# Optimization experiments

Measured on AMD Instinct MI355X. Metric: run time of the kernel, lower is better.

## Reference

```python
import jax, jax.numpy as jnp
import numpy as np
import math
from jax import lax

HIDDEN = 512
BETA = 1.0
MAX_ITERATIONS = 5
CONV_THRESH = 1e-4
SCALE = BETA / math.sqrt(HIDDEN)


def setup_inputs() -> dict:
    key = jax.random.key(0)
    ks = jax.random.split(key, 9)
    B, S, H = 4, 2048, HIDDEN
    w = 1.0 / math.sqrt(H)  # roughly nn.Linear init scale
    return {
        "x": jax.random.normal(ks[0], (B, S, H), jnp.float32),
        "Wq": jax.random.normal(ks[1], (H, H), jnp.float32) * w,
        "bq": jax.random.normal(ks[2], (H,), jnp.float32) * w,
        "Wk": jax.random.normal(ks[3], (H, H), jnp.float32) * w,
        "bk": jax.random.normal(ks[4], (H,), jnp.float32) * w,
        "Wv": jax.random.normal(ks[5], (H, H), jnp.float32) * w,
        "bv": jax.random.normal(ks[6], (H,), jnp.float32) * w,
        "Wo": jax.random.normal(ks[7], (H, H), jnp.float32) * w,
        "bo": jax.random.normal(ks[8], (H,), jnp.float32) * w,
    }


def _hopfield_update(state, keys):
    # scores: [B, S, S]
    scores = jnp.einsum('bsh,bth->bst', state, keys) * SCALE
    attn = jax.nn.softmax(scores, axis=-1)
    return jnp.einsum('bst,bth->bsh', attn, keys)


def reference(x, Wq, bq, Wk, bk, Wv, bv, Wo, bo):
    query = x @ Wq.T + bq
    keys = x @ Wk.T + bk
    values = x @ Wv.T + bv

    # Iterative Hopfield loop: torch breaks after the update that converges.
    # We run a fixed-length scan, freezing state once converged (same math).
    def step(carry, _):
        state, converged, iters = carry
        new_state = _hopfield_update(state, keys)
        # global Frobenius norms, matching torch.norm over the whole tensor
        delta = jnp.linalg.norm(new_state - state) / (jnp.linalg.norm(state) + 1e-8)
        active = jnp.logical_not(converged)
        state = jnp.where(active, new_state, state)
        iters = iters + active.astype(jnp.int32)
        converged = converged | (active & (delta < CONV_THRESH))
        return (state, converged, iters), None

    init = (query, jnp.array(False), jnp.array(0, jnp.int32))
    (state, converged, iterations), _ = lax.scan(step, init, None, length=MAX_ITERATIONS)

    # Final readout attention against values
    scores = jnp.einsum('bsh,bth->bst', state, keys) * SCALE
    attn = jax.nn.softmax(scores, axis=-1)
    out = jnp.einsum('bst,bth->bsh', attn, values)
    out = out @ Wo.T + bo  # dropout p=0.0 / eval: identity
    return out, iterations, converged
```

## Files before the change

kernel.cpp:

```cpp
#include <hip/hip_runtime.h>
#include <hip/hip_bf16.h>
#include <math.h>

#define HH 512
#define BB 4
#define SS 2048
#define NN (BB*SS)
#define SCALE_F 0.04419417382415922f
#define THRESH 1e-4f
#define CTL_FLOATS 1024

typedef __attribute__((ext_vector_type(8))) short bf16x8;
typedef __attribute__((ext_vector_type(4))) float f32x4;

struct Ctl { float sum_d; float sum_o; int iters; int conv; int cur; int bf[10]; };

__device__ __forceinline__ float b2f(unsigned short u) {
    union { unsigned int i; float f; } c; c.i = ((unsigned int)u) << 16; return c.f;
}
__device__ __forceinline__ unsigned short f2b(float f) {
    unsigned int x = __float_as_uint(f);
    unsigned int r = (x + 0x7FFFu + ((x >> 16) & 1u)) >> 16;
    return (unsigned short)r;
}
__device__ __forceinline__ void splitf(float x, unsigned short& h, unsigned short& l) {
    h = f2b(x);
    l = f2b(x - b2f(h));
}
__device__ __forceinline__ f32x4 MF(bf16x8 a, bf16x8 b, f32x4 c) {
    return __builtin_amdgcn_mfma_f32_16x16x32_bf16(a, b, c, 0, 0, 0);
}

typedef __attribute__((address_space(1))) const unsigned int gu32;
typedef __attribute__((address_space(3))) unsigned int lu32;
__device__ __forceinline__ void gl_lds16(const unsigned short* g, unsigned short* l) {
    __builtin_amdgcn_global_load_lds((gu32*)g, (lu32*)l, 16, 0, 0);
}

#define SBAR() do { \
    asm volatile("s_waitcnt vmcnt(0) lgkmcnt(0)" ::: "memory"); \
    __builtin_amdgcn_s_barrier(); \
    asm volatile("" ::: "memory"); \
} while (0)
#define FBAR() do { \
    asm volatile("s_waitcnt lgkmcnt(0)" ::: "memory"); \
    __builtin_amdgcn_s_barrier(); \
    asm volatile("" ::: "memory"); \
} while (0)

__global__ __launch_bounds__(256) void detect_dtypes(
        const void* p0, const void* p1, const void* p2, const void* p3, const void* p4,
        const void* p5, const void* p6, const void* p7, const void* p8, Ctl* sc)
{
    const void* ps[9] = {p0,p1,p2,p3,p4,p5,p6,p7,p8};
    const int   ns[9] = {NN*HH, HH*HH, HH, HH*HH, HH, HH*HH, HH, HH*HH, HH};
    const int i = blockIdx.x;
    const unsigned short* u = (const unsigned short*)ps[i];
    const int n = ns[i] < 4096 ? ns[i] : 4096;
    __shared__ int cnt;
    if (threadIdx.x == 0) cnt = 0;
    __syncthreads();
    int c = 0;
    for (int j = threadIdx.x; j < n; j += 256) {
        const int e = (u[j] >> 7) & 0xFF;
        if (e < 32 || e >= 224) ++c;
    }
    if (c) atomicAdd(&cnt, c);
    __syncthreads();
    if (threadIdx.x == 0) sc->bf[i] = (cnt * 16 < n) ? 1 : 0;
}

__global__ __launch_bounds__(64) void init_flags(Ctl* sc) {
    if (threadIdx.x == 0) {
        sc->iters = 0; sc->conv = 0; sc->cur = 0; sc->sum_d = 0.f; sc->sum_o = 0.f;
        int any = 0;
        for (int i = 0; i < 9; ++i) any |= sc->bf[i];
        sc->bf[9] = any;
    }
}

__global__ __launch_bounds__(256) void mfma_gemm(
    const void* __restrict__ Xv, int xIdx,
    const void* __restrict__ Wv, int wIdx,
    const void* __restrict__ Bv, int bIdx,
    float* __restrict__ outF, void* __restrict__ outExt,
    unsigned short* __restrict__ pKH, unsigned short* __restrict__ pKL,
    unsigned short* __restrict__ pKTH, unsigned short* __restrict__ pKTL,
    float* __restrict__ S0w, float* __restrict__ S1w,
    int mode, const Ctl* __restrict__ sc)
{
    __shared__ unsigned short Xh[64][72], Xl[64][72], Wh[64][72], Wl[64][72];
    const int tid = threadIdx.x;
    const int cur = sc->cur;
    const void* Xp = (xIdx == -2) ? (const void*)(cur ? S1w : S0w) : Xv;
    const bool xbf = (xIdx >= 0) && (sc->bf[xIdx] != 0);
    const bool wbf = (sc->bf[wIdx] != 0);
    const bool bbf = (sc->bf[bIdx] != 0);
    const bool obf = (mode == 1) && (sc->bf[9] != 0);
    const bool xs = !xbf, ws = !wbf;

    const int m0 = blockIdx.x * 64, n0 = blockIdx.y * 64;
    const int lane = tid & 63, w = tid >> 6;
    const int mi = w & 1, ni = w >> 1;
    const int quad = lane >> 4, l16 = lane & 15;
    const int srow = tid >> 2, skb = (tid & 3) * 16;

    f32x4 acc[2][2];
    #pragma unroll
    for (int a = 0; a < 2; ++a)
        #pragma unroll
        for (int bq = 0; bq < 2; ++bq) acc[a][bq] = (f32x4){0.f, 0.f, 0.f, 0.f};

    for (int kc = 0; kc < HH; kc += 64) {
        __syncthreads();
        {
            float v[16];
            if (xbf) {
                const unsigned short* p = (const unsigned short*)Xp + (size_t)(m0 + srow)*HH + kc + skb;
                #pragma unroll
                for (int i = 0; i < 4; ++i) {
                    ushort4 t = *(const ushort4*)(p + 4*i);
                    v[4*i]=b2f(t.x); v[4*i+1]=b2f(t.y); v[4*i+2]=b2f(t.z); v[4*i+3]=b2f(t.w);
                }
            } else {
                const float* p = (const float*)Xp + (size_t)(m0 + srow)*HH + kc + skb;
                #pragma unroll
                for (int i = 0; i < 4; ++i) {
                    float4 t = *(const float4*)(p + 4*i);
                    v[4*i]=t.x; v[4*i+1]=t.y; v[4*i+2]=t.z; v[4*i+3]=t.w;
                }
            }
            #pragma unroll
            for (int i = 0; i < 4; ++i) {
                unsigned short h[4], l[4];
                #pragma unroll
                for (int j = 0; j < 4; ++j) splitf(v[4*i+j], h[j], l[j]);
                *(ushort4*)&Xh[srow][skb + 4*i] = make_ushort4(h[0], h[1], h[2], h[3]);
                if (xs) *(ushort4*)&Xl[srow][skb + 4*i] = make_ushort4(l[0], l[1], l[2], l[3]);
            }
        }
        {
            float v[16];
            if (wbf) {
                const unsigned short* p = (const unsigned short*)Wv + (size_t)(n0 + srow)*HH + kc + skb;
                #pragma unroll
                for (int i = 0; i < 4; ++i) {
                    ushort4 t = *(const ushort4*)(p + 4*i);
                    v[4*i]=b2f(t.x); v[4*i+1]=b2f(t.y); v[4*i+2]=b2f(t.z); v[4*i+3]=b2f(t.w);
                }
            } else {
                const float* p = (const float*)Wv + (size_t)(n0 + srow)*HH + kc + skb;
                #pragma unroll
                for (int i = 0; i < 4; ++i) {
                    float4 t = *(const float4*)(p + 4*i);
                    v[4*i]=t.x; v[4*i+1]=t.y; v[4*i+2]=t.z; v[4*i+3]=t.w;
                }
            }
            #pragma unroll
            for (int i = 0; i < 4; ++i) {
                unsigned short h[4], l[4];
                #pragma unroll
                for (int j = 0; j < 4; ++j) splitf(v[4*i+j], h[j], l[j]);
                *(ushort4*)&Wh[srow][skb + 4*i] = make_ushort4(h[0], h[1], h[2], h[3]);
                if (ws) *(ushort4*)&Wl[srow][skb + 4*i] = make_ushort4(l[0], l[1], l[2], l[3]);
            }
        }
        __syncthreads();
        #pragma unroll
        for (int d = 0; d < 2; ++d) {
            const int kl = 32*d + quad*8;
            #pragma unroll
            for (int mt = 0; mt < 2; ++mt) {
                const int xr = 32*mi + 16*mt + l16;
                bf16x8 ahx = *(const bf16x8*)&Xh[xr][kl];
                bf16x8 alx;
                if (xs) alx = *(const bf16x8*)&Xl[xr][kl];
                #pragma unroll
                for (int nt = 0; nt < 2; ++nt) {
                    const int wr = 32*ni + 16*nt + l16;
                    bf16x8 bh = *(const bf16x8*)&Wh[wr][kl];
                    acc[mt][nt] = MF(ahx, bh, acc[mt][nt]);
                    if (xs) acc[mt][nt] = MF(alx, bh, acc[mt][nt]);
                    if (ws) {
                        bf16x8 bl = *(const bf16x8*)&Wl[wr][kl];
                        acc[mt][nt] = MF(ahx, bl, acc[mt][nt]);
                    }
                }
            }
        }
    }
    unsigned short* vtH = nullptr;
    if (mode == 4) { vtH = (unsigned short*)(cur ? S0w : S1w); }
    #pragma unroll
    for (int nt = 0; nt < 2; ++nt) {
        const int col = n0 + 32*ni + 16*nt + l16;
        const float bv = bbf ? b2f(((const unsigned short*)Bv)[col]) : ((const float*)Bv)[col];
        #pragma unroll
        for (int mt = 0; mt < 2; ++mt)
            #pragma unroll
            for (int e = 0; e < 4; ++e) {
                const int row = m0 + 32*mi + 16*mt + quad*4 + e;
                const float vv = acc[mt][nt][e] + bv;
                const size_t idx = (size_t)row*HH + col;
                if (mode == 0) outF[idx] = vv;
                else if (mode == 1) {
                    if (obf) ((unsigned short*)outExt)[idx] = f2b(vv);
                    else     ((float*)outExt)[idx] = vv;
                } else {
                    unsigned short h, l; splitf(vv, h, l);
                    const size_t t = ((size_t)(row >> 11) * HH + col) * SS + (row & 2047);
                    if (mode == 3) {
                        pKH[idx] = h; pKL[idx] = l;
                        pKTH[t] = h;  pKTL[t] = l;
                    } else {
                        vtH[t] = h; vtH[(size_t)NN*HH + t] = l;
                    }
                }
            }
    }
}

template<bool FINAL>
__global__ __launch_bounds__(512, 2) void mfma_attn(
    float* __restrict__ S0w, float* __restrict__ S1w,
    const unsigned short* __restrict__ KH, const unsigned short* __restrict__ KL,
    const unsigned short* __restrict__ KTH, const unsigned short* __restrict__ KTL,
    Ctl* sc)
{
    if constexpr (!FINAL) { if (sc->conv) return; }
    const int cur = sc->cur;
    float* Scur = cur ? S1w : S0w;
    float* Out  = FINAL ? Scur : (cur ? S0w : S1w);
    const unsigned short* VTH = FINAL ? (const unsigned short*)(cur ? S0w : S1w) : KTH;
    const unsigned short* VTL = FINAL ? (VTH + (size_t)NN*HH) : KTL;

    __shared__ __align__(16) unsigned short UB0[16384];
    __shared__ __align__(16) unsigned short UB1[16384];
    __shared__ __align__(16) unsigned short SHl[32*520];
    __shared__ __align__(16) unsigned short Pth[32*72], Ptl[32*72];
    __shared__ __align__(16) float Sld[32*68];
    __shared__ __align__(16) float mld[32], lld[32], ald[32];
    __shared__ float redd[8], redo[8];

    const int tid = threadIdx.x;
    const int lane = tid & 63, w = tid >> 6;
    const int quad = lane >> 4, l16 = lane & 15;
    const int r = w & 1, s = w >> 1;

    const int bid = blockIdx.x;
    const int e8 = bid & 7;
    const int b = e8 >> 1;
    const int q0 = 32 * ((bid >> 3) + 32 * (e8 & 1));

    const size_t bSSHH = (size_t)b * SS * HH;
    const size_t bHHSS = (size_t)b * HH * SS;

    const int keyS = 4*w + quad;
    const int swS  = ((lane & 15) ^ (keyS & 7)) * 8;
    const int r3   = lane >> 3;
    const int swP  = ((lane & 7) ^ (r3 & 7)) * 8;
    const int rowP = 8*w + r3;
    const int hidP0 = 128*(rowP >> 5) + (rowP & 31);
    const int hidP1 = 128*(2 + (rowP >> 5)) + (rowP & 31);

    auto stageS = [&](int c, int kt, unsigned short* ub) {
        const size_t g0 = bSSHH + (size_t)(kt*64 + keyS)*HH + c*128 + swS;
        const size_t g1 = bSSHH + (size_t)(kt*64 + keyS + 32)*HH + c*128 + swS;
        gl_lds16(KH + g0, ub +                 w*64*8);
        gl_lds16(KH + g1, ub +        4096 +   w*64*8);
        gl_lds16(KL + g0, ub + 8192 +          w*64*8);
        gl_lds16(KL + g1, ub + 8192 + 4096 +   w*64*8);
    };
    auto stageP = [&](int c, int kt, unsigned short* ub) {
        const size_t g0 = bHHSS + (size_t)(hidP0 + 32*c)*SS + (size_t)kt*64 + swP;
        const size_t g1 = bHHSS + (size_t)(hidP1 + 32*c)*SS + (size_t)kt*64 + swP;
        gl_lds16(VTH + g0, ub +                 w*64*8);
        gl_lds16(VTH + g1, ub +        4096 +   w*64*8);
        gl_lds16(VTL + g0, ub + 8192 +          w*64*8);
        gl_lds16(VTL + g1, ub + 8192 + 4096 +   w*64*8);
    };

    stageS(0, 0, UB0);

    bf16x8 ah[16];
    {
        const float* Qr = Scur + ((size_t)b*SS + q0 + 16*r + l16) * HH + quad*8;
        #pragma unroll
        for (int f = 0; f < 16; ++f) {
            float4 v0 = *(const float4*)(Qr + 32*f);
            float4 v1 = *(const float4*)(Qr + 32*f + 4);
            unsigned short h[8], l[8];
            splitf(v0.x,h[0],l[0]); splitf(v0.y,h[1],l[1]); splitf(v0.z,h[2],l[2]); splitf(v0.w,h[3],l[3]);
            splitf(v1.x,h[4],l[4]); splitf(v1.y,h[5],l[5]); splitf(v1.z,h[6],l[6]); splitf(v1.w,h[7],l[7]);
            bf16x8 af;
            #pragma unroll
            for (int j = 0; j < 8; ++j) af[j] = (short)h[j];
            ah[f] = af;
            if (s == 0) {
                unsigned short* d = &SHl[(16*r + l16)*520 + 32*f + quad*8];
                *(ushort4*)(d)     = make_ushort4(l[0], l[1], l[2], l[3]);
                *(ushort4*)(d + 4) = make_ushort4(l[4], l[5], l[6], l[7]);
            }
        }
        if (tid < 32) { mld[tid] = -INFINITY; lld[tid] = 0.f; }
    }

    f32x4 O[8];
    #pragma unroll
    for (int i = 0; i < 8; ++i) O[i] = (f32x4){0.f, 0.f, 0.f, 0.f};

    const int shlbase = (16*r + l16)*520 + quad*8;

    for (int kt = 0; kt < SS/64; ++kt) {
        f32x4 sA = (f32x4){0.f,0.f,0.f,0.f}, sB = (f32x4){0.f,0.f,0.f,0.f};
        #pragma unroll
        for (int c = 0; c < 4; ++c) {
            unsigned short* ub = (c & 1) ? UB1 : UB0;
            SBAR();
            if (c < 3) stageS(c+1, kt, (c & 1) ? UB0 : UB1);
            else       stageP(0, kt, UB0);
            #pragma unroll
            for (int kf = 0; kf < 4; ++kf) {
                bf16x8 alf = *(const bf16x8*)&SHl[shlbase + c*128 + kf*32];
                const int cc = ((4*kf + quad) ^ (l16 & 7)) * 8;
                bf16x8 bh = *(const bf16x8*)&ub[(16*s + l16)*128 + cc];
                bf16x8 bl = *(const bf16x8*)&ub[8192 + (16*s + l16)*128 + cc];
                const bf16x8 a = ah[c*4 + kf];
                if (kf & 1) {
                    sB = MF(a, bh, sB); sB = MF(alf, bh, sB); sB = MF(a, bl, sB);
                } else {
                    sA = MF(a, bh, sA); sA = MF(alf, bh, sA); sA = MF(a, bl, sA);
                }
            }
        }
        f32x4 sacc = sA + sB;
        #pragma unroll
        for (int e = 0; e < 4; ++e)
            Sld[(16*r + quad*4 + e)*68 + 16*s + l16] = sacc[e] * SCALE_F;
        FBAR();
        {
            const int row = tid >> 4, sg = tid & 15;
            const float* sr = Sld + row*68 + sg*4;
            float4 x0 = *(const float4*)(sr);
            float mt = fmaxf(fmaxf(x0.x, x0.y), fmaxf(x0.z, x0.w));
            #pragma unroll
            for (int mk = 1; mk < 16; mk <<= 1) mt = fmaxf(mt, __shfl_xor(mt, mk, 16));
            const float mprev = mld[row];
            const float mnew = fmaxf(mprev, mt);
            float p[4];
            p[0]=__expf(x0.x-mnew); p[1]=__expf(x0.y-mnew); p[2]=__expf(x0.z-mnew); p[3]=__expf(x0.w-mnew);
            float ps = p[0]+p[1]+p[2]+p[3];
            #pragma unroll
            for (int mk = 1; mk < 16; mk <<= 1) ps += __shfl_xor(ps, mk, 16);
            const float alpha = __expf(mprev - mnew);
            if (sg == 0) { mld[row] = mnew; lld[row] = lld[row]*alpha + ps; ald[row] = alpha; }
            unsigned short h[4], l[4];
            #pragma unroll
            for (int i = 0; i < 4; ++i) splitf(p[i], h[i], l[i]);
            *(ushort4*)&Pth[row*72 + sg*4] = make_ushort4(h[0],h[1],h[2],h[3]);
            *(ushort4*)&Ptl[row*72 + sg*4] = make_ushort4(l[0],l[1],l[2],l[3]);
        }
        FBAR();
        {
            const float4 av = *(const float4*)&ald[16*r + 4*quad];
            const float a4[4] = {av.x, av.y, av.z, av.w};
            #pragma unroll
            for (int i = 0; i < 8; ++i)
                #pragma unroll
                for (int e = 0; e < 4; ++e) O[i][e] *= a4[e];
        }
        bf16x8 pah[2], pal[2];
        #pragma unroll
        for (int kf = 0; kf < 2; ++kf) {
            pah[kf] = *(const bf16x8*)&Pth[(16*r + l16)*72 + kf*32 + quad*8];
            pal[kf] = *(const bf16x8*)&Ptl[(16*r + l16)*72 + kf*32 + quad*8];
        }
        #pragma unroll
        for (int c = 0; c < 4; ++c) {
            unsigned short* ub = (c & 1) ? UB1 : UB0;
            SBAR();
            if (c < 3)              stageP(c+1, kt, (c & 1) ? UB0 : UB1);
            else if (kt+1 < SS/64)  stageS(0, kt+1, UB0);
            #pragma unroll
            for (int nt = 0; nt < 2; ++nt) {
                const int rb = (32*s + 16*nt + l16)*64;
                #pragma unroll
                for (int kf = 0; kf < 2; ++kf) {
                    const int cc = ((4*kf + quad) ^ (l16 & 7)) * 8;
                    bf16x8 bh = *(const bf16x8*)&ub[rb + cc];
                    bf16x8 bl = *(const bf16x8*)&ub[8192 + rb + cc];
                    O[c*2+nt] = MF(pah[kf], bh, O[c*2+nt]);
                    O[c*2+nt] = MF(pal[kf], bh, O[c*2+nt]);
                    O[c*2+nt] = MF(pah[kf], bl, O[c*2+nt]);
                }
            }
        }
    }
    const float4 lv = *(const float4*)&lld[16*r + 4*quad];
    const float inv[4] = {1.f/lv.x, 1.f/lv.y, 1.f/lv.z, 1.f/lv.w};
    float pd = 0.f, po2 = 0.f;
    #pragma unroll
    for (int c = 0; c < 4; ++c)
        #pragma unroll
        for (int nt = 0; nt < 2; ++nt)
            #pragma unroll
            for (int e = 0; e < 4; ++e) {
                const int row = q0 + 16*r + quad*4 + e;
                const int col = 128*s + 32*c + 16*nt + l16;
                const float nv = O[c*2+nt][e] * inv[e];
                const size_t idx = (size_t)b*SS*HH + (size_t)row*HH + col;
                if constexpr (!FINAL) {
                    const float old = Scur[idx];
                    const float d = nv - old;
                    pd += d*d; po2 += old*old;
                }
                Out[idx] = nv;
            }
    if constexpr (!FINAL) {
        #pragma unroll
        for (int mk = 1; mk < 64; mk <<= 1) {
            pd  += __shfl_xor(pd, mk, 64);
            po2 += __shfl_xor(po2, mk, 64);
        }
        if (lane == 0) { redd[w] = pd; redo[w] = po2; }
        __syncthreads();
        if (tid == 0) {
            float td = 0.f, to = 0.f;
            #pragma unroll
            for (int i = 0; i < 8; ++i) { td += redd[i]; to += redo[i]; }
            atomicAdd(&sc->sum_d, td);
            atomicAdd(&sc->sum_o, to);
        }
    }
}

__global__ __launch_bounds__(64) void flag_update(Ctl* sc) {
    if (threadIdx.x != 0) return;
    if (sc->conv) return;
    sc->cur ^= 1;
    sc->iters += 1;
    const float delta = sqrtf(sc->sum_d) / (sqrtf(sc->sum_o) + 1e-8f);
    if (delta < THRESH) sc->conv = 1;
    sc->sum_d = 0.f; sc->sum_o = 0.f;
}

__global__ __launch_bounds__(64) void write_scalars(const Ctl* sc, void* outv) {
    if (threadIdx.x != 0) return;
    if (sc->bf[9]) {
        unsigned short* o = (unsigned short*)outv;
        o[(size_t)NN*HH]     = f2b((float)sc->iters);
        o[(size_t)NN*HH + 1] = f2b(sc->conv ? 1.0f : 0.0f);
    } else {
        float* o = (float*)outv;
        o[(size_t)NN*HH]     = (float)sc->iters;
        o[(size_t)NN*HH + 1] = sc->conv ? 1.0f : 0.0f;
    }
}

extern "C" void kernel_launch(void* const* d_in, const int* in_sizes, int n_in,
                              void* d_out, int out_size, void* d_ws, size_t ws_size,
                              hipStream_t stream)
{
    const void* x  = d_in[0];
    const void* Wq = d_in[1];
    const void* bq = d_in[2];
    const void* Wk = d_in[3];
    const void* bk = d_in[4];
    const void* Wv = d_in[5];
    const void* bv = d_in[6];
    const void* Wo = d_in[7];
    const void* bo = d_in[8];

    Ctl* sc = (Ctl*)d_ws;
    float* S0 = (float*)d_ws + CTL_FLOATS;
    float* S1 = S0 + (size_t)NN*HH;
    unsigned short* KH  = (unsigned short*)(S1 + (size_t)NN*HH);
    unsigned short* KL  = KH  + (size_t)NN*HH;
    unsigned short* KTH = KL  + (size_t)NN*HH;
    unsigned short* KTL = KTH + (size_t)NN*HH;

    const dim3 ggrid(NN/64, HH/64);
    const int  agrid = 256;

    detect_dtypes<<<9, 256, 0, stream>>>(x, Wq, bq, Wk, bk, Wv, bv, Wo, bo, sc);
    init_flags<<<1, 64, 0, stream>>>(sc);

    mfma_gemm<<<ggrid, 256, 0, stream>>>(x, 0, Wq, 1, bq, 2, S0, nullptr,
                                         nullptr, nullptr, nullptr, nullptr, S0, S1, 0, sc);
    mfma_gemm<<<ggrid, 256, 0, stream>>>(x, 0, Wk, 3, bk, 4, nullptr, nullptr,
                                         KH, KL, KTH, KTL, S0, S1, 3, sc);

    for (int it = 0; it < 5; ++it) {
        mfma_attn<false><<<agrid, 512, 0, stream>>>(S0, S1, KH, KL, KTH, KTL, sc);
        flag_update<<<1, 64, 0, stream>>>(sc);
    }

    mfma_gemm<<<ggrid, 256, 0, stream>>>(x, 0, Wv, 5, bv, 6, nullptr, nullptr,
                                         nullptr, nullptr, nullptr, nullptr, S0, S1, 4, sc);
    mfma_attn<true><<<agrid, 512, 0, stream>>>(S0, S1, KH, KL, KTH, KTL, sc);
    mfma_gemm<<<ggrid, 256, 0, stream>>>(nullptr, -2, Wo, 7, bo, 8, nullptr, d_out,
                                         nullptr, nullptr, nullptr, nullptr, S0, S1, 1, sc);
    if (out_size >= (int)((size_t)NN*HH + 2))
        write_scalars<<<1, 64, 0, stream>>>(sc, d_out);
}
```

Before: 1.577 ms.

## Triple-buffer K/V LDS staging with prefetch distance two and partial vmcnt waits

Replaces the double-buffered LDS staging of K and V tiles with a three-buffer ring. Each step now prefetches two chunks ahead and waits only until the older loads have landed (vmcnt(4)), not for all loads. The goal is to hide global-to-LDS latency behind the MFMA work. It costs 32KB more LDS per block, which may lower occupancy under launch_bounds(512,2), and it issues redundant wraparound loads on the last iteration.

Result: slower. 1.881 ms (+19.3%).

```diff
diff --git a/kernel.cpp b/kernel.cpp
--- a/kernel.cpp
+++ b/kernel.cpp
@@ -37,8 +37,8 @@
     __builtin_amdgcn_global_load_lds((gu32*)g, (lu32*)l, 16, 0, 0);
 }
 
-#define SBAR() do { \
-    asm volatile("s_waitcnt vmcnt(0) lgkmcnt(0)" ::: "memory"); \
+#define WBAR() do { \
+    asm volatile("s_waitcnt vmcnt(4) lgkmcnt(0)" ::: "memory"); \
     __builtin_amdgcn_s_barrier(); \
     asm volatile("" ::: "memory"); \
 } while (0)
@@ -234,8 +234,7 @@
     const unsigned short* VTH = FINAL ? (const unsigned short*)(cur ? S0w : S1w) : KTH;
     const unsigned short* VTL = FINAL ? (VTH + (size_t)NN*HH) : KTL;
 
-    __shared__ __align__(16) unsigned short UB0[16384];
-    __shared__ __align__(16) unsigned short UB1[16384];
+    __shared__ __align__(16) unsigned short UB[3*16384];
     __shared__ __align__(16) unsigned short SHl[32*520];
     __shared__ __align__(16) unsigned short Pth[32*72], Ptl[32*72];
     __shared__ __align__(16) float Sld[32*68];
@@ -280,8 +279,6 @@
         gl_lds16(VTL + g1, ub + 8192 + 4096 +   w*64*8);
     };
 
-    stageS(0, 0, UB0);
-
     bf16x8 ah[16];
     {
         const float* Qr = Scur + ((size_t)b*SS + q0 + 16*r + l16) * HH + quad*8;
@@ -305,20 +302,28 @@
         if (tid < 32) { mld[tid] = -INFINITY; lld[tid] = 0.f; }
     }
 
+    stageS(0, 0, UB);
+    stageS(1, 0, UB + 16384);
+
     f32x4 O[8];
     #pragma unroll
     for (int i = 0; i < 8; ++i) O[i] = (f32x4){0.f, 0.f, 0.f, 0.f};
 
     const int shlbase = (16*r + l16)*520 + quad*8;
 
+    int cb = 0;
     for (int kt = 0; kt < SS/64; ++kt) {
         f32x4 sA = (f32x4){0.f,0.f,0.f,0.f}, sB = (f32x4){0.f,0.f,0.f,0.f};
         #pragma unroll
         for (int c = 0; c < 4; ++c) {
-            unsigned short* ub = (c & 1) ? UB1 : UB0;
-            SBAR();
-            if (c < 3) stageS(c+1, kt, (c & 1) ? UB0 : UB1);
-            else       stageP(0, kt, UB0);
+            unsigned short* ub = UB + cb*16384;
+            WBAR();
+            {
+                int tb = cb + 2; if (tb >= 3) tb -= 3;
+                unsigned short* tu = UB + tb*16384;
+                if (c < 2) stageS(c+2, kt, tu);
+                else       stageP(c-2, kt, tu);
+            }
             #pragma unroll
             for (int kf = 0; kf < 4; ++kf) {
                 bf16x8 alf = *(const bf16x8*)&SHl[shlbase + c*128 + kf*32];
@@ -332,6 +337,7 @@
                     sA = MF(a, bh, sA); sA = MF(alf, bh, sA); sA = MF(a, bl, sA);
                 }
             }
+            cb = cb + 1; if (cb >= 3) cb = 0;
         }
         f32x4 sacc = sA + sB;
         #pragma unroll
@@ -377,10 +383,17 @@
         }
         #pragma unroll
         for (int c = 0; c < 4; ++c) {
-            unsigned short* ub = (c & 1) ? UB1 : UB0;
-            SBAR();
-            if (c < 3)              stageP(c+1, kt, (c & 1) ? UB0 : UB1);
-            else if (kt+1 < SS/64)  stageS(0, kt+1, UB0);
+            unsigned short* ub = UB + cb*16384;
+            WBAR();
+            {
+                int tb = cb + 2; if (tb >= 3) tb -= 3;
+                unsigned short* tu = UB + tb*16384;
+                if (c < 2) stageP(c+2, kt, tu);
+                else {
+                    int ktn = kt + 1; if (ktn >= SS/64) ktn = 0;
+                    stageS(c-2, ktn, tu);
+                }
+            }
             #pragma unroll
             for (int nt = 0; nt < 2; ++nt) {
                 const int rb = (32*s + 16*nt + l16)*64;
@@ -394,6 +407,7 @@
                     O[c*2+nt] = MF(pah[kf], bl, O[c*2+nt]);
                 }
             }
+            cb = cb + 1; if (cb >= 3) cb = 0;
         }
     }
     const float4 lv = *(const float4*)&lld[16*r + 4*quad];
```
